# Optimization experiments

Hardware: AMD Instinct MI355X
Metric: run time of the kernel (lower is better)

## Reference

```python
import jax, jax.numpy as jnp
import numpy as np

D = 2048      # d_model
QH = 32       # query heads
KVH = 8       # kv heads
HD = D // QH  # head_dim = 64
B = 2
S = 2048
THETA = 1000000.0


def _rope_cos_sin(seq_len, hd, dtype):
    inv_freq = 1.0 / (THETA ** (jnp.arange(0, hd, 2, dtype=jnp.float32) / hd))
    t = jnp.arange(seq_len, dtype=jnp.float32)
    freqs = jnp.einsum('i,j->ij', t, inv_freq)          # [S, hd/2]
    emb = jnp.concatenate([freqs, freqs], axis=-1)      # [S, hd]
    cos = jnp.cos(emb)[None, :, None, :].astype(dtype)  # [1,S,1,hd]
    sin = jnp.sin(emb)[None, :, None, :].astype(dtype)
    return cos, sin


def _rotate_half(x):
    half = x.shape[-1] // 2
    x1, x2 = x[..., :half], x[..., half:]
    return jnp.concatenate([-x2, x1], axis=-1)


def setup_inputs() -> dict:
    key = jax.random.key(0)
    ks = jax.random.split(key, 9)
    inp = {
        'q': jax.random.normal(ks[0], (B, S, D), dtype=jnp.float32),
        'k': jax.random.normal(ks[1], (B, S, D), dtype=jnp.float32),
        'v': jax.random.normal(ks[2], (B, S, D), dtype=jnp.float32),
        'attn_mask': jnp.ones((B, S), dtype=jnp.float32),  # ignored by source math
        'Wq': jax.random.normal(ks[3], (D, D), dtype=jnp.float32) * 0.02,
        'Wk': jax.random.normal(ks[4], (D, KVH * HD), dtype=jnp.float32) * 0.02,
        'Wv': jax.random.normal(ks[5], (D, KVH * HD), dtype=jnp.float32) * 0.02,
        'Wo': jax.random.normal(ks[6], (D, D), dtype=jnp.float32) * 0.02,
        'bo': jnp.zeros((D,), dtype=jnp.float32),
    }
    return inp


def reference(q, k, v, attn_mask, Wq, Wk, Wv, Wo, bo):
    b, s, _ = q.shape
    qh = (q @ Wq).reshape(b, s, QH, HD)
    kh = (k @ Wk).reshape(b, s, KVH, HD)
    vh = (v @ Wv).reshape(b, s, KVH, HD)

    cos, sin = _rope_cos_sin(s, HD, qh.dtype)
    qh = qh * cos + _rotate_half(qh) * sin
    kh = kh * cos + _rotate_half(kh) * sin

    g = QH // KVH
    # torch .repeat tiles the head axis: [h0..h7, h0..h7, ...]
    kh = jnp.tile(kh, (1, 1, g, 1))  # [b,s,QH,HD]
    vh = jnp.tile(vh, (1, 1, g, 1))

    qt = qh.transpose(0, 2, 1, 3)  # [b,QH,s,HD]
    kt = kh.transpose(0, 2, 1, 3)
    vt = vh.transpose(0, 2, 1, 3)

    scale = 1.0 / jnp.sqrt(jnp.asarray(HD, dtype=qt.dtype))
    scores = jnp.einsum('bhqd,bhkd->bhqk', qt, kt) * scale
    # source passes attn_mask=None, is_causal=False when a mask is given:
    # full non-causal attention, mask value unused.
    attn = jax.nn.softmax(scores, axis=-1)
    out = jnp.einsum('bhqk,bhkd->bhqd', attn, vt)
    out = out.transpose(0, 2, 1, 3).reshape(b, s, D)
    return out @ Wo + bo
```

## Files before the change

kernel.cpp:

```cpp
#include <hip/hip_runtime.h>
#include <math.h>

#define D_    2048
#define QH_   32
#define KVH_  8
#define HD_   64
#define B_    2
#define S_    2048
#define NROW_ (B_*S_)
#define KVD_  (KVH_*HD_)
#define LOG2E 1.44269504f

typedef __bf16 bf16;
typedef __bf16 bf16x2 __attribute__((ext_vector_type(2)));
typedef __bf16 bf16x4 __attribute__((ext_vector_type(4)));
typedef __bf16 bf16x8 __attribute__((ext_vector_type(8)));
typedef float  f32x4  __attribute__((ext_vector_type(4)));
typedef float  f32x16 __attribute__((ext_vector_type(16)));

__device__ __forceinline__ f32x4 mfma16(bf16x8 a, bf16x8 b, f32x4 c) {
  return __builtin_amdgcn_mfma_f32_16x16x32_bf16(a, b, c, 0, 0, 0);
}
__device__ __forceinline__ f32x16 mfma32(bf16x8 a, bf16x8 b, f32x16 c) {
  return __builtin_amdgcn_mfma_f32_32x32x16_bf16(a, b, c, 0, 0, 0);
}

__device__ __forceinline__ void gload_lds16(const bf16* g, bf16* l) {
  __builtin_amdgcn_global_load_lds(
      (const __attribute__((address_space(1))) void*)g,
      (__attribute__((address_space(3))) void*)l, 16, 0, 0);
}

__device__ __forceinline__ unsigned pack_bf16(float a, float b) {
  union { bf16x2 v; unsigned u; } t;
  t.v[0] = (bf16)a; t.v[1] = (bf16)b;
  return t.u;
}

__global__ void k_ropetab(float2* __restrict__ tab) {
  int idx = blockIdx.x * 256 + threadIdx.x;
  int s = idx >> 5, d = idx & 31;
  float invf = exp2f(-(float)d * 0.62286151f);
  float ang = (float)s * invf;
  float sn, cs;
  sincosf(ang, &sn, &cs);
  tab[idx] = make_float2(cs, sn);
}

__global__ void k_convert(const float* __restrict__ in, bf16* __restrict__ out, int n4) {
  int i = blockIdx.x * 256 + threadIdx.x;
  if (i >= n4) return;
  f32x4 v = ((const f32x4*)in)[i];
  bf16x4 o;
#pragma unroll
  for (int j = 0; j < 4; j++) o[j] = (bf16)v[j];
  ((bf16x4*)out)[i] = o;
}

__global__ void k_convert2(const float* __restrict__ in0, const float* __restrict__ in1,
                           bf16* __restrict__ o0, bf16* __restrict__ o1, int n4) {
  const float* in = blockIdx.z ? in1 : in0;
  bf16* out = blockIdx.z ? o1 : o0;
  int i = blockIdx.x * 256 + threadIdx.x;
  if (i >= n4) return;
  f32x4 v = ((const f32x4*)in)[i];
  bf16x4 o;
#pragma unroll
  for (int j = 0; j < 4; j++) o[j] = (bf16)v[j];
  ((bf16x4*)out)[i] = o;
}

__device__ __forceinline__ void transpose_w_body(const float* W, bf16* Wt, int K, int N) {
  __shared__ float tile[32][33];
  int n0 = blockIdx.x * 32, k0 = blockIdx.y * 32;
  int tx = threadIdx.x, ty = threadIdx.y;
#pragma unroll
  for (int j = 0; j < 4; j++)
    tile[ty + 8*j][tx] = W[(size_t)(k0 + ty + 8*j) * N + n0 + tx];
  __syncthreads();
#pragma unroll
  for (int j = 0; j < 4; j++)
    Wt[(size_t)(n0 + ty + 8*j) * K + k0 + tx] = (bf16)tile[tx][ty + 8*j];
}

__global__ void k_transpose_w(const float* __restrict__ W, bf16* __restrict__ Wt,
                              int K, int N) {
  transpose_w_body(W, Wt, K, N);
}

__global__ void k_transpose_w2(const float* __restrict__ W0, const float* __restrict__ W1,
                               bf16* __restrict__ T0, bf16* __restrict__ T1) {
  transpose_w_body(blockIdx.z ? W1 : W0, blockIdx.z ? T1 : T0, D_, KVD_);
}

template<int EPI>
__device__ __forceinline__ void gemm_body(bf16* Asb, bf16* Bsb,
                                          const bf16* A, const bf16* Bt, void* Cout,
                                          const float* bias, const float2* tab,
                                          int M, int N, int K) {
  int tid = threadIdx.x;
  int wave = tid >> 6, lane = tid & 63, hi = lane >> 4, lr = lane & 15;
  int wm = wave >> 1, wn = wave & 1;
  int m0 = blockIdx.y * 128, n0 = blockIdx.x * 128;
  f32x4 acc[4][4] = {};
  int nk = K >> 6;

  int s_row[4], s_dch[4];
#pragma unroll
  for (int i = 0; i < 4; i++) {
    int c = i * 256 + tid;
    s_row[i] = c >> 3;
    s_dch[i] = (c & 7) ^ (s_row[i] & 7);
  }

#define GSTAGE(buf, kt_)                                                       \
  do {                                                                         \
    int k0_ = (kt_) * 64;                                                      \
    _Pragma("unroll")                                                          \
    for (int i = 0; i < 4; i++) {                                              \
      gload_lds16(A  + (size_t)(m0 + s_row[i]) * K + k0_ + s_dch[i] * 8,       \
                  Asb + ((buf) * 8192 + (i * 256 + wave * 64) * 8));           \
      gload_lds16(Bt + (size_t)(n0 + s_row[i]) * K + k0_ + s_dch[i] * 8,       \
                  Bsb + ((buf) * 8192 + (i * 256 + wave * 64) * 8));           \
    }                                                                          \
  } while (0)

  GSTAGE(0, 0);
  __syncthreads();

  for (int kt = 0; kt < nk; kt++) {
    int cur = kt & 1;
    if (kt + 1 < nk) GSTAGE(cur ^ 1, kt + 1);
#pragma unroll
    for (int kk = 0; kk < 2; kk++) {
      bf16x8 af[4], bfr[4];
#pragma unroll
      for (int mt = 0; mt < 4; mt++) {
        int row = wm * 64 + mt * 16 + lr;
        int sl = (kk * 4 + hi) ^ (row & 7);
        af[mt] = *(const bf16x8*)(Asb + cur * 8192 + row * 64 + sl * 8);
      }
#pragma unroll
      for (int nt = 0; nt < 4; nt++) {
        int row = wn * 64 + nt * 16 + lr;
        int sl = (kk * 4 + hi) ^ (row & 7);
        bfr[nt] = *(const bf16x8*)(Bsb + cur * 8192 + row * 64 + sl * 8);
      }
      __builtin_amdgcn_s_setprio(1);
#pragma unroll
      for (int mt = 0; mt < 4; mt++)
#pragma unroll
        for (int nt = 0; nt < 4; nt++)
          acc[mt][nt] = mfma16(af[mt], bfr[nt], acc[mt][nt]);
      __builtin_amdgcn_s_setprio(0);
    }
    __syncthreads();
  }
#undef GSTAGE

  if (EPI == 1) {
#pragma unroll
    for (int mt = 0; mt < 4; mt++)
#pragma unroll
      for (int r = 0; r < 4; r++) {
        int grow = m0 + wm * 64 + mt * 16 + 4 * hi + r;
        int s = grow & (S_ - 1);
#pragma unroll
        for (int nt = 0; nt < 2; nt++) {
          int gcol = n0 + wn * 64 + nt * 16 + lr;
          float2 cs = tab[s * 32 + nt * 16 + lr];
          float x1 = acc[mt][nt][r], x2 = acc[mt][nt + 2][r];
          ((bf16*)Cout)[(size_t)grow * N + gcol]      = (bf16)(x1 * cs.x - x2 * cs.y);
          ((bf16*)Cout)[(size_t)grow * N + gcol + 32] = (bf16)(x2 * cs.x + x1 * cs.y);
        }
      }
  } else {
#pragma unroll
    for (int mt = 0; mt < 4; mt++)
#pragma unroll
      for (int nt = 0; nt < 4; nt++)
#pragma unroll
        for (int r = 0; r < 4; r++) {
          int grow = m0 + wm * 64 + mt * 16 + 4 * hi + r;
          int gcol = n0 + wn * 64 + nt * 16 + lr;
          ((float*)Cout)[(size_t)grow * N + gcol] = acc[mt][nt][r] + bias[gcol];
        }
  }
}

__global__ __launch_bounds__(256) void k_gemm_q(const bf16* __restrict__ A,
                                                const bf16* __restrict__ Bt,
                                                bf16* __restrict__ C,
                                                const float2* __restrict__ tab) {
  __shared__ alignas(16) bf16 As[2][128 * 64];
  __shared__ alignas(16) bf16 Bs[2][128 * 64];
  gemm_body<1>(&As[0][0], &Bs[0][0], A, Bt, C, nullptr, tab, NROW_, D_, D_);
}

__global__ __launch_bounds__(256) void k_gemm_o(const bf16* __restrict__ A,
                                                const bf16* __restrict__ Bt,
                                                float* __restrict__ C,
                                                const float* __restrict__ bias) {
  __shared__ alignas(16) bf16 As[2][128 * 64];
  __shared__ alignas(16) bf16 Bs[2][128 * 64];
  gemm_body<2>(&As[0][0], &Bs[0][0], A, Bt, C, bias, nullptr, NROW_, D_, D_);
}

template<int EPI>
__device__ __forceinline__ void gemm_body64(bf16* Asb, bf16* Bsb,
                                            const bf16* A, const bf16* Bt, void* Cout,
                                            const float2* tab) {
  const int K = D_, N = KVD_;
  int tid = threadIdx.x;
  int wave = tid >> 6, lane = tid & 63, hi = lane >> 4, lr = lane & 15;
  int m0 = blockIdx.y * 64, n0 = blockIdx.x * 128;
  int nbase = (wave >> 1) * 64 + (wave & 1) * 16;
  f32x4 acc[4][2] = {};
  const int nk = K >> 6;

  int a_row[2], a_dch[2], b_row[4], b_dch[4];
#pragma unroll
  for (int i = 0; i < 2; i++) {
    int c = i * 256 + tid;
    a_row[i] = c >> 3;
    a_dch[i] = (c & 7) ^ (a_row[i] & 7);
  }
#pragma unroll
  for (int i = 0; i < 4; i++) {
    int c = i * 256 + tid;
    b_row[i] = c >> 3;
    b_dch[i] = (c & 7) ^ (b_row[i] & 7);
  }

#define GSTAGE64(buf, kt_)                                                     \
  do {                                                                         \
    int k0_ = (kt_) * 64;                                                      \
    _Pragma("unroll")                                                          \
    for (int i = 0; i < 2; i++)                                                \
      gload_lds16(A + (size_t)(m0 + a_row[i]) * K + k0_ + a_dch[i] * 8,        \
                  Asb + ((buf) * 4096 + (i * 256 + wave * 64) * 8));           \
    _Pragma("unroll")                                                          \
    for (int i = 0; i < 4; i++)                                                \
      gload_lds16(Bt + (size_t)(n0 + b_row[i]) * K + k0_ + b_dch[i] * 8,       \
                  Bsb + ((buf) * 8192 + (i * 256 + wave * 64) * 8));           \
  } while (0)

  GSTAGE64(0, 0);
  __syncthreads();

  for (int kt = 0; kt < nk; kt++) {
    int cur = kt & 1;
    if (kt + 1 < nk) GSTAGE64(cur ^ 1, kt + 1);
#pragma unroll
    for (int kk = 0; kk < 2; kk++) {
      bf16x8 af[4], bfr[2];
#pragma unroll
      for (int mt = 0; mt < 4; mt++) {
        int row = mt * 16 + lr;
        int sl = (kk * 4 + hi) ^ (row & 7);
        af[mt] = *(const bf16x8*)(Asb + cur * 4096 + row * 64 + sl * 8);
      }
#pragma unroll
      for (int nt = 0; nt < 2; nt++) {
        int row = nbase + nt * 32 + lr;
        int sl = (kk * 4 + hi) ^ (row & 7);
        bfr[nt] = *(const bf16x8*)(Bsb + cur * 8192 + row * 64 + sl * 8);
      }
      __builtin_amdgcn_s_setprio(1);
#pragma unroll
      for (int mt = 0; mt < 4; mt++)
#pragma unroll
        for (int nt = 0; nt < 2; nt++) {
          if (EPI == 3) acc[mt][nt] = mfma16(bfr[nt], af[mt], acc[mt][nt]);
          else          acc[mt][nt] = mfma16(af[mt], bfr[nt], acc[mt][nt]);
        }
      __builtin_amdgcn_s_setprio(0);
    }
    __syncthreads();
  }
#undef GSTAGE64

  if (EPI == 1) {
#pragma unroll
    for (int mt = 0; mt < 4; mt++)
#pragma unroll
      for (int r = 0; r < 4; r++) {
        int grow = m0 + mt * 16 + 4 * hi + r;
        int s = grow & (S_ - 1);
        int d = (wave & 1) * 16 + lr;
        int gcol = n0 + nbase + lr;
        float2 cs = tab[s * 32 + d];
        float x1 = acc[mt][0][r], x2 = acc[mt][1][r];
        ((bf16*)Cout)[(size_t)grow * N + gcol]      = (bf16)(x1 * cs.x - x2 * cs.y);
        ((bf16*)Cout)[(size_t)grow * N + gcol + 32] = (bf16)(x2 * cs.x + x1 * cs.y);
      }
  } else {
    int b = m0 >> 11;
#pragma unroll
    for (int mt = 0; mt < 4; mt++)
#pragma unroll
      for (int nt = 0; nt < 2; nt++)
#pragma unroll
        for (int r = 0; r < 4; r++) {
          int n = n0 + nbase + nt * 32 + 4 * hi + r;
          int m = m0 + mt * 16 + lr;
          ((bf16*)Cout)[((size_t)(b * KVD_ + n)) * S_ + (m & (S_ - 1))] =
              (bf16)acc[mt][nt][r];
        }
  }
}

__global__ __launch_bounds__(256) void k_gemm_kv(const bf16* __restrict__ A0,
                                                 const bf16* __restrict__ A1,
                                                 const bf16* __restrict__ B0,
                                                 const bf16* __restrict__ B1,
                                                 bf16* __restrict__ Kh,
                                                 bf16* __restrict__ Vt,
                                                 const float2* __restrict__ tab) {
  __shared__ alignas(16) bf16 As[2][64 * 64];
  __shared__ alignas(16) bf16 Bs[2][128 * 64];
  if (blockIdx.z == 0) gemm_body64<1>(&As[0][0], &Bs[0][0], A0, B0, Kh, tab);
  else                 gemm_body64<3>(&As[0][0], &Bs[0][0], A1, B1, Vt, nullptr);
}

__global__ __launch_bounds__(512, 4) void k_attn(const bf16* __restrict__ Qh,
                                                 const bf16* __restrict__ Kh,
                                                 const bf16* __restrict__ Vt,
                                                 bf16* __restrict__ ctx) {
  __shared__ alignas(16) bf16 Ks[2][64 * 64];
  __shared__ alignas(16) bf16 Vs[2][64 * 64];
  int tid = threadIdx.x;
  int wave = tid >> 6, lane = tid & 63, hi2 = lane >> 5, l31 = lane & 31;
  int qt = blockIdx.x, h = blockIdx.y, b = blockIdx.z;
  int kv = h & 7;
  int q0 = qt * 256 + wave * 32;

  bf16x8 qf[4];
  {
    const float QSC = 0.125f * LOG2E;
    const bf16* qp = Qh + (size_t)(b * S_ + q0 + l31) * D_ + h * HD_ + hi2 * 8;
#pragma unroll
    for (int df = 0; df < 4; df++) {
      bf16x8 v = *(const bf16x8*)(qp + 16 * df);
#pragma unroll
      for (int j = 0; j < 8; j++) v[j] = (bf16)((float)v[j] * QSC);
      qf[df] = v;
    }
  }

  f32x16 o0, o1, accl;
#pragma unroll
  for (int i = 0; i < 16; i++) { o0[i] = 0.f; o1[i] = 0.f; accl[i] = 0.f; }
  bf16x8 ones;
#pragma unroll
  for (int j = 0; j < 8; j++) ones[j] = (bf16)1.0f;

  const bf16* Kg = Kh + (size_t)(b * S_) * KVD_ + kv * HD_;
  const bf16* Vg = Vt + (size_t)(b * KVH_ + kv) * HD_ * S_;

  int c_row = tid >> 3, c_slot = tid & 7;
  int c_dch = c_slot ^ (c_row & 7);

#define STAGE(buf, kt_)                                                        \
  do {                                                                         \
    gload_lds16(Kg + (size_t)((kt_) * 64 + c_row) * KVD_ + c_dch * 8,          \
                &Ks[buf][tid * 8]);                                            \
    gload_lds16(Vg + (size_t)c_row * S_ + (kt_) * 64 + c_dch * 8,              \
                &Vs[buf][tid * 8]);                                            \
  } while (0)

  STAGE(0, 0);
  __syncthreads();

  const int NT = S_ / 64;
  for (int kt = 0; kt < NT; kt++) {
    int cur = kt & 1;
    if (kt + 1 < NT) STAGE(cur ^ 1, kt + 1);

    const bf16* Kb = &Ks[cur][0];
    const bf16* Vb = &Vs[cur][0];

    f32x16 s0, s1;
#pragma unroll
    for (int i = 0; i < 16; i++) { s0[i] = 0.f; s1[i] = 0.f; }
    __builtin_amdgcn_s_setprio(1);
#pragma unroll
    for (int df = 0; df < 4; df++) {
      int ch = hi2 + 2 * df;
      int sl = (ch ^ (l31 & 7)) << 3;
      bf16x8 k0 = *(const bf16x8*)(Kb + l31 * 64 + sl);
      bf16x8 k1 = *(const bf16x8*)(Kb + (l31 + 32) * 64 + sl);
      s0 = mfma32(k0, qf[df], s0);
      s1 = mfma32(k1, qf[df], s1);
    }
    __builtin_amdgcn_s_setprio(0);

#pragma unroll
    for (int i = 0; i < 16; i++) s0[i] = __builtin_amdgcn_exp2f(s0[i]);
#pragma unroll
    for (int i = 0; i < 16; i++) s1[i] = __builtin_amdgcn_exp2f(s1[i]);

    unsigned Rk[2][4][2];
#pragma unroll
    for (int m = 0; m < 4; m++)
#pragma unroll
      for (int w = 0; w < 2; w++) {
        Rk[0][m][w] = pack_bf16(s0[4*m + 2*w], s0[4*m + 2*w + 1]);
        Rk[1][m][w] = pack_bf16(s1[4*m + 2*w], s1[4*m + 2*w + 1]);
      }
#pragma unroll
    for (int kf = 0; kf < 2; kf++)
#pragma unroll
      for (int kp = 0; kp < 2; kp++)
#pragma unroll
        for (int w = 0; w < 2; w++)
          asm volatile("v_permlane32_swap_b32 %0, %1"
                       : "+v"(Rk[kf][2*kp][w]), "+v"(Rk[kf][2*kp+1][w]));
    bf16x8 pf[4];
#pragma unroll
    for (int kfr = 0; kfr < 4; kfr++) {
      int kf = kfr >> 1, k2 = (kfr & 1) * 2;
      union { unsigned d[4]; bf16x8 v; } u;
      u.d[0] = Rk[kf][k2][0];     u.d[1] = Rk[kf][k2][1];
      u.d[2] = Rk[kf][k2 + 1][0]; u.d[3] = Rk[kf][k2 + 1][1];
      pf[kfr] = u.v;
    }

    __builtin_amdgcn_s_setprio(1);
#pragma unroll
    for (int kfr = 0; kfr < 4; kfr++) {
      int ch = hi2 + 2 * kfr;
      int sl = (ch ^ (l31 & 7)) << 3;
      bf16x8 v0 = *(const bf16x8*)(Vb + l31 * 64 + sl);
      bf16x8 v1 = *(const bf16x8*)(Vb + (l31 + 32) * 64 + sl);
      o0 = mfma32(pf[kfr], v0, o0);
      o1 = mfma32(pf[kfr], v1, o1);
      accl = mfma32(pf[kfr], ones, accl);
    }
    __builtin_amdgcn_s_setprio(0);
    __syncthreads();
  }
#undef STAGE

#pragma unroll
  for (int r = 0; r < 16; r++) {
    int rowq = (r & 3) + 8 * (r >> 2) + 4 * hi2;
    float inv = 1.f / accl[r];
    size_t base = (size_t)(b * S_ + q0 + rowq) * D_ + h * HD_;
    ctx[base + l31]      = (bf16)(o0[r] * inv);
    ctx[base + l31 + 32] = (bf16)(o1[r] * inv);
  }
}

extern "C" void kernel_launch(void* const* d_in, const int* in_sizes, int n_in,
                              void* d_out, int out_size, void* d_ws, size_t ws_size,
                              hipStream_t stream) {
  const float* q  = (const float*)d_in[0];
  const float* k  = (const float*)d_in[1];
  const float* v  = (const float*)d_in[2];
  const float* Wq = (const float*)d_in[4];
  const float* Wk = (const float*)d_in[5];
  const float* Wv = (const float*)d_in[6];
  const float* Wo = (const float*)d_in[7];
  const float* bo = (const float*)d_in[8];

  char* ws = (char*)d_ws;
  bf16*   A0  = (bf16*)(ws + 0);
  bf16*   A1  = (bf16*)(ws + 16777216);
  bf16*   Wt  = (bf16*)(ws + 33554432);
  bf16*   Qh  = (bf16*)(ws + 41943040);
  bf16*   Kh  = (bf16*)(ws + 58720256);
  bf16*   Vt  = (bf16*)(ws + 62914560);
  float2* tab = (float2*)(ws + 67108864);
  bf16*   WtK = Wt;
  bf16*   WtV = (bf16*)(ws + 33554432 + 2097152);
  bf16*   ctx = A1;

  const int n4 = NROW_ * D_ / 4;

  k_ropetab<<<(S_ * 32) / 256, 256, 0, stream>>>(tab);
  k_convert<<<n4 / 256, 256, 0, stream>>>(q, A0, n4);
  k_transpose_w<<<dim3(D_/32, D_/32), dim3(32, 8), 0, stream>>>(Wq, Wt, D_, D_);
  k_gemm_q<<<dim3(D_/128, NROW_/128), 256, 0, stream>>>(A0, Wt, Qh, tab);
  k_convert2<<<dim3(n4 / 256, 1, 2), 256, 0, stream>>>(k, v, A0, A1, n4);
  k_transpose_w2<<<dim3(KVD_/32, D_/32, 2), dim3(32, 8), 0, stream>>>(Wk, Wv, WtK, WtV);
  k_gemm_kv<<<dim3(KVD_/128, NROW_/64, 2), 256, 0, stream>>>(A0, A1, WtK, WtV, Kh, Vt, tab);
  k_attn<<<dim3(S_/256, QH_, B_), 512, 0, stream>>>(Qh, Kh, Vt, ctx);
  k_transpose_w<<<dim3(D_/32, D_/32), dim3(32, 8), 0, stream>>>(Wo, Wt, D_, D_);
  k_gemm_o<<<dim3(D_/128, NROW_/128), 256, 0, stream>>>(ctx, Wt, (float*)d_out, bo);
}
```

Measured before the change: 256.7 us.

## Fuse fp32-to-bf16 conversion of k/v into the KV projection GEMM

Removes the separate k/v conversion kernel and has the KV GEMM load fp32 activations directly. It converts them to bf16 in registers and writes them into shared memory, with the loads issued one tile ahead. This eliminates a full read/write pass over the k and v activations and one kernel launch. The cost is twice the bytes per A tile load, repeated across column blocks, and a register-staged path in place of direct global-to-LDS loads.

```diff
diff --git a/kernel.cpp b/kernel.cpp
--- a/kernel.cpp
+++ b/kernel.cpp
@@ -48,19 +48,6 @@
 }
 
 __global__ void k_convert(const float* __restrict__ in, bf16* __restrict__ out, int n4) {
-  int i = blockIdx.x * 256 + threadIdx.x;
-  if (i >= n4) return;
-  f32x4 v = ((const f32x4*)in)[i];
-  bf16x4 o;
-#pragma unroll
-  for (int j = 0; j < 4; j++) o[j] = (bf16)v[j];
-  ((bf16x4*)out)[i] = o;
-}
-
-__global__ void k_convert2(const float* __restrict__ in0, const float* __restrict__ in1,
-                           bf16* __restrict__ o0, bf16* __restrict__ o1, int n4) {
-  const float* in = blockIdx.z ? in1 : in0;
-  bf16* out = blockIdx.z ? o1 : o0;
   int i = blockIdx.x * 256 + threadIdx.x;
   if (i >= n4) return;
   f32x4 v = ((const f32x4*)in)[i];
@@ -208,7 +195,7 @@
 
 template<int EPI>
 __device__ __forceinline__ void gemm_body64(bf16* Asb, bf16* Bsb,
-                                            const bf16* A, const bf16* Bt, void* Cout,
+                                            const float* Af, const bf16* Bt, void* Cout,
                                             const float2* tab) {
   const int K = D_, N = KVD_;
   int tid = threadIdx.x;
@@ -232,25 +219,53 @@
     b_dch[i] = (c & 7) ^ (b_row[i] & 7);
   }
 
-#define GSTAGE64(buf, kt_)                                                     \
+  f32x4 areg[2][2];
+
+#define A_LOAD(kt_)                                                            \
   do {                                                                         \
     int k0_ = (kt_) * 64;                                                      \
     _Pragma("unroll")                                                          \
-    for (int i = 0; i < 2; i++)                                                \
-      gload_lds16(A + (size_t)(m0 + a_row[i]) * K + k0_ + a_dch[i] * 8,        \
-                  Asb + ((buf) * 4096 + (i * 256 + wave * 64) * 8));           \
+    for (int i = 0; i < 2; i++) {                                              \
+      const float* p = Af + (size_t)(m0 + a_row[i]) * K + k0_ + a_dch[i] * 8;  \
+      areg[i][0] = *(const f32x4*)p;                                           \
+      areg[i][1] = *(const f32x4*)(p + 4);                                     \
+    }                                                                          \
+  } while (0)
+
+#define A_WRITE(buf)                                                           \
+  do {                                                                         \
+    _Pragma("unroll")                                                          \
+    for (int i = 0; i < 2; i++) {                                              \
+      bf16x8 v;                                                                \
+      _Pragma("unroll")                                                        \
+      for (int j = 0; j < 4; j++) {                                            \
+        v[j]     = (bf16)areg[i][0][j];                                        \
+        v[4 + j] = (bf16)areg[i][1][j];                                        \
+      }                                                                        \
+      *(bf16x8*)(Asb + (buf) * 4096 + (i * 256 + tid) * 8) = v;                \
+    }                                                                          \
+  } while (0)
+
+#define GSTAGE_B(buf, kt_)                                                     \
+  do {                                                                         \
+    int k0_ = (kt_) * 64;                                                      \
     _Pragma("unroll")                                                          \
     for (int i = 0; i < 4; i++)                                                \
       gload_lds16(Bt + (size_t)(n0 + b_row[i]) * K + k0_ + b_dch[i] * 8,       \
                   Bsb + ((buf) * 8192 + (i * 256 + wave * 64) * 8));           \
   } while (0)
 
-  GSTAGE64(0, 0);
+  A_LOAD(0);
+  GSTAGE_B(0, 0);
+  A_WRITE(0);
   __syncthreads();
 
   for (int kt = 0; kt < nk; kt++) {
     int cur = kt & 1;
-    if (kt + 1 < nk) GSTAGE64(cur ^ 1, kt + 1);
+    if (kt + 1 < nk) {
+      A_LOAD(kt + 1);
+      GSTAGE_B(cur ^ 1, kt + 1);
+    }
 #pragma unroll
     for (int kk = 0; kk < 2; kk++) {
       bf16x8 af[4], bfr[2];
@@ -276,9 +291,12 @@
         }
       __builtin_amdgcn_s_setprio(0);
     }
+    if (kt + 1 < nk) A_WRITE(cur ^ 1);
     __syncthreads();
   }
-#undef GSTAGE64
+#undef A_LOAD
+#undef A_WRITE
+#undef GSTAGE_B
 
   if (EPI == 1) {
 #pragma unroll
@@ -310,8 +328,8 @@
   }
 }
 
-__global__ __launch_bounds__(256) void k_gemm_kv(const bf16* __restrict__ A0,
-                                                 const bf16* __restrict__ A1,
+__global__ __launch_bounds__(256) void k_gemm_kv(const float* __restrict__ kf,
+                                                 const float* __restrict__ vf,
                                                  const bf16* __restrict__ B0,
                                                  const bf16* __restrict__ B1,
                                                  bf16* __restrict__ Kh,
@@ -319,8 +337,8 @@
                                                  const float2* __restrict__ tab) {
   __shared__ alignas(16) bf16 As[2][64 * 64];
   __shared__ alignas(16) bf16 Bs[2][128 * 64];
-  if (blockIdx.z == 0) gemm_body64<1>(&As[0][0], &Bs[0][0], A0, B0, Kh, tab);
-  else                 gemm_body64<3>(&As[0][0], &Bs[0][0], A1, B1, Vt, nullptr);
+  if (blockIdx.z == 0) gemm_body64<1>(&As[0][0], &Bs[0][0], kf, B0, Kh, tab);
+  else                 gemm_body64<3>(&As[0][0], &Bs[0][0], vf, B1, Vt, nullptr);
 }
 
 __global__ __launch_bounds__(512, 4) void k_attn(const bf16* __restrict__ Qh,
@@ -482,9 +500,8 @@
   k_convert<<<n4 / 256, 256, 0, stream>>>(q, A0, n4);
   k_transpose_w<<<dim3(D_/32, D_/32), dim3(32, 8), 0, stream>>>(Wq, Wt, D_, D_);
   k_gemm_q<<<dim3(D_/128, NROW_/128), 256, 0, stream>>>(A0, Wt, Qh, tab);
-  k_convert2<<<dim3(n4 / 256, 1, 2), 256, 0, stream>>>(k, v, A0, A1, n4);
   k_transpose_w2<<<dim3(KVD_/32, D_/32, 2), dim3(32, 8), 0, stream>>>(Wk, Wv, WtK, WtV);
-  k_gemm_kv<<<dim3(KVD_/128, NROW_/64, 2), 256, 0, stream>>>(A0, A1, WtK, WtV, Kh, Vt, tab);
+  k_gemm_kv<<<dim3(KVD_/128, NROW_/64, 2), 256, 0, stream>>>(k, v, WtK, WtV, Kh, Vt, tab);
   k_attn<<<dim3(S_/256, QH_, B_), 512, 0, stream>>>(Qh, Kh, Vt, ctx);
   k_transpose_w<<<dim3(D_/32, D_/32), dim3(32, 8), 0, stream>>>(Wo, Wt, D_, D_);
   k_gemm_o<<<dim3(D_/128, NROW_/128), 256, 0, stream>>>(ctx, Wt, (float*)d_out, bo);
```

New measurement: 244.1 us. -4.9%, faster.
